# Kernel optimization log

Measured on AMD Instinct MI355X. Metric: run time of the kernel, lower is better.

## Reference

```python
import jax, jax.numpy as jnp
import numpy as np

B, N, DIM = 4, 2048, 512
H, DH = 8, 64  # n_heads, dim_head; inner = H*DH = 512
SCALE = DH ** -0.5


def setup_inputs() -> dict:
    key = jax.random.key(0)
    k1, k2, k3 = jax.random.split(key, 3)
    inner = H * DH
    X = jax.random.normal(k1, (B, N, DIM), dtype=jnp.float32)
    W_qkv = jax.random.normal(k2, (DIM, 3 * inner), dtype=jnp.float32) * (DIM ** -0.5)
    W_out = jax.random.normal(k3, (inner, DIM), dtype=jnp.float32) * (inner ** -0.5)
    b_out = jnp.zeros((DIM,), dtype=jnp.float32)
    return {"X": X, "W_qkv": W_qkv, "W_out": W_out, "b_out": b_out}


def reference(X, W_qkv, W_out, b_out):
    # X: (b, n, dim)
    qkv = X @ W_qkv                      # (b, n, 3*h*d)
    q, k, v = jnp.split(qkv, 3, axis=-1)
    def to_heads(t):
        b, n, _ = t.shape
        return t.reshape(b, n, H, DH).transpose(0, 2, 1, 3)  # (b, h, n, d)
    q, k, v = to_heads(q), to_heads(k), to_heads(v)
    # NOTE: original computes scores[n, m] = k_n . q_m and softmaxes over m (query axis)
    scores = jnp.einsum('bhnd,bhmd->bhnm', k, q) * SCALE     # (b, h, n_k, m_q)
    att = jax.nn.softmax(scores, axis=-1)
    # out token axis is the KEY index n: out[n, d] = sum_e att[n, e] * v[e, d]
    out = jnp.einsum('bhne,bhed->bhnd', att, v)              # (b, h, n, d)
    out = out.transpose(0, 2, 1, 3).reshape(X.shape[0], X.shape[1], H * DH)  # (b, n, h*d)
    return out @ W_out + b_out
```

## Files before the change

### kernel.cpp

```cpp
#include <hip/hip_runtime.h>
#include <hip/hip_bf16.h>

typedef __bf16 bf16_t;
typedef bf16_t bf16x8 __attribute__((ext_vector_type(8)));
typedef bf16_t bf16x4v __attribute__((ext_vector_type(4)));
typedef float f32x4 __attribute__((ext_vector_type(4)));
typedef float f32x16 __attribute__((ext_vector_type(16)));
typedef int i32x4 __attribute__((ext_vector_type(4)));

#define B_SZ 4
#define N_TOK 2048
#define DIM 512
#define H_N 8
#define DH 64
#define INNER 512
#define M_ROWS 8192
#define NQKV 1536
#define K_FOLD 0.18033688011112042f

#define GLD_LDS16(gp, lp)                                          \
  __builtin_amdgcn_global_load_lds(                                \
      (const __attribute__((address_space(1))) void*)(gp),         \
      (__attribute__((address_space(3))) void*)(lp), 16, 0, 0)

__device__ __forceinline__ float fexp2(float x) {
#if __has_builtin(__builtin_amdgcn_exp2f)
  return __builtin_amdgcn_exp2f(x);
#else
  float r;
  asm volatile("v_exp_f32 %0, %1\n\ts_nop 1" : "=v"(r) : "v"(x));
  return r;
#endif
}

__device__ __forceinline__ int cvtpk_bf16(float lo, float hi) {
  int r;
  asm("v_cvt_pk_bf16_f32 %0, %1, %2" : "=v"(r) : "v"(lo), "v"(hi));
  return r;
}

__device__ __forceinline__ void permswap32(int& a, int& b) {
  asm volatile("v_permlane32_swap_b32 %0, %1" : "+v"(a), "+v"(b));
}


__global__ void f32_to_bf16_kernel(const float* __restrict__ src,
                                   bf16_t* __restrict__ dst, int n4) {
  int i = blockIdx.x * blockDim.x + threadIdx.x;
  int stride = gridDim.x * blockDim.x;
  for (; i < n4; i += stride) {
    float4 f = reinterpret_cast<const float4*>(src)[i];
    bf16x4v o;
    o.x = (bf16_t)f.x; o.y = (bf16_t)f.y; o.z = (bf16_t)f.z; o.w = (bf16_t)f.w;
    reinterpret_cast<bf16x4v*>(dst)[i] = o;
  }
}

__global__ void transpose_f32_to_bf16_kernel(const float* __restrict__ src,
                                             bf16_t* __restrict__ dst, int R, int C) {
  int t = blockIdx.x * blockDim.x + threadIdx.x;
  if (t >= R * C) return;
  int r = t / C, c = t - r * C;
  dst[(size_t)c * R + r] = (bf16_t)src[t];
}

template <int MODE>
__global__ __launch_bounds__(256) void gemm_bf16_kernel(
    const bf16_t* __restrict__ A, const bf16_t* __restrict__ Bt,
    int M, int Nn, int K,
    bf16_t* __restrict__ qb, bf16_t* __restrict__ kb, bf16_t* __restrict__ vtb,
    float* __restrict__ outF, const float* __restrict__ bias) {
  __shared__ bf16_t As[128 * 64];
  __shared__ bf16_t Bs[128 * 64];

  const int tid = threadIdx.x;
  const int lane = tid & 63;
  const int wave = tid >> 6;
  const int g = lane >> 4, c = lane & 15;
  const int wm = (wave >> 1) * 64, wn = (wave & 1) * 64;
  const int m0 = blockIdx.x * 128, n0 = blockIdx.y * 128;

  f32x4 acc[4][4] = {};

  for (int k0 = 0; k0 < K; k0 += 64) {
    __syncthreads();
    #pragma unroll
    for (int i = 0; i < 4; ++i) {
      int blk = i * 256 + tid;
      int row = blk >> 3;
      int cb = (blk & 7) ^ (row & 7);
      int base = (i * 256 + wave * 64) * 8;
      GLD_LDS16(A + (size_t)(m0 + row) * K + k0 + cb * 8, &As[base]);
      GLD_LDS16(Bt + (size_t)(n0 + row) * K + k0 + cb * 8, &Bs[base]);
    }
    __syncthreads();
    __builtin_amdgcn_s_setprio(1);
    #pragma unroll
    for (int ks = 0; ks < 2; ++ks) {
      bf16x8 af[4], bfr[4];
      #pragma unroll
      for (int i = 0; i < 4; ++i) {
        af[i] = *reinterpret_cast<const bf16x8*>(
            &As[(wm + i * 16 + c) * 64 + (((ks * 4 + g) ^ (c & 7)) * 8)]);
        bfr[i] = *reinterpret_cast<const bf16x8*>(
            &Bs[(wn + i * 16 + c) * 64 + (((ks * 4 + g) ^ (c & 7)) * 8)]);
      }
      #pragma unroll
      for (int mi = 0; mi < 4; ++mi)
        #pragma unroll
        for (int ni = 0; ni < 4; ++ni)
          acc[mi][ni] = __builtin_amdgcn_mfma_f32_16x16x32_bf16(
              af[mi], bfr[ni], acc[mi][ni], 0, 0, 0);
    }
    __builtin_amdgcn_s_setprio(0);
  }

  #pragma unroll
  for (int mi = 0; mi < 4; ++mi) {
    #pragma unroll
    for (int ni = 0; ni < 4; ++ni) {
      int colg = n0 + wn + ni * 16 + c;
      if (MODE == 0) {
        int s = colg >> 9;
        int hh = (colg >> 6) & 7, dd = colg & 63;
        int rowg0 = m0 + wm + mi * 16 + g * 4;
        int bb = rowg0 >> 11, nn = rowg0 & 2047;
        if (s == 2) {
          bf16x4v pk;
          pk.x = (bf16_t)acc[mi][ni][0];
          pk.y = (bf16_t)acc[mi][ni][1];
          pk.z = (bf16_t)acc[mi][ni][2];
          pk.w = (bf16_t)acc[mi][ni][3];
          *reinterpret_cast<bf16x4v*>(
              &vtb[(((size_t)(bb * H_N + hh)) * DH + dd) * N_TOK + nn]) = pk;
        } else {
          float sc = (s == 1) ? K_FOLD : 1.0f;
          bf16_t* dst = (s == 0) ? qb : kb;
          #pragma unroll
          for (int r = 0; r < 4; ++r)
            dst[(((size_t)(bb * H_N + hh)) * N_TOK + nn + r) * DH + dd] =
                (bf16_t)(acc[mi][ni][r] * sc);
        }
      } else {
        #pragma unroll
        for (int r = 0; r < 4; ++r) {
          int rowg = m0 + wm + mi * 16 + g * 4 + r;
          outF[(size_t)rowg * Nn + colg] = acc[mi][ni][r] + bias[colg];
        }
      }
    }
  }
}

__global__ __launch_bounds__(256, 1) void attn_kernel(
    const bf16_t* __restrict__ Qproj, const bf16_t* __restrict__ Kproj,
    const bf16_t* __restrict__ Vt, bf16_t* __restrict__ att_out) {
  const int glin = blockIdx.x;
  const int xcd = glin & 7;
  const int jj = glin >> 3;
  const int hb = xcd * 4 + (jj >> 3);
  const int rb = jj & 7;
  const int h = hb & 7, b = hb >> 3;

  const size_t hbo = (size_t)(b * H_N + h);
  const bf16_t* Aq = Kproj + hbo * N_TOK * DH;
  const bf16_t* Ak = Qproj + hbo * N_TOK * DH;
  const bf16_t* Av = Vt + hbo * (size_t)DH * N_TOK;

  const int tid = threadIdx.x, lane = tid & 63, wave = tid >> 6;
  const int nl = lane & 31;
  const int hf = lane >> 5;
  const int r0 = rb * 256, wr0 = wave * 64;

  __shared__ bf16_t sK[2][128 * 64];
  __shared__ bf16_t sV[2][64 * 128];

  bf16x8 qreg[2][4];
  #pragma unroll
  for (int cs = 0; cs < 2; ++cs)
    #pragma unroll
    for (int ks = 0; ks < 4; ++ks)
      qreg[cs][ks] = *reinterpret_cast<const bf16x8*>(
          &Aq[(size_t)(r0 + wr0 + cs * 32 + nl) * DH + ks * 16 + hf * 8]);

  f32x16 accO[2][2] = {};
  float Lp[2][2] = {};

  auto stage = [&](bf16_t* dK, bf16_t* dV, int j0) {
    #pragma unroll
    for (int i = 0; i < 4; ++i) {
      int idx = i * 256 + tid;
      int base = (i * 256 + wave * 64) * 8;
      int rowK = idx >> 3;
      int cbK = (idx & 7) ^ (rowK & 7);
      GLD_LDS16(Ak + (size_t)(j0 + rowK) * DH + cbK * 8, dK + base);
      int rowV = idx >> 4;
      int sv = idx & 15;
      int pV = (sv & 8) | ((sv & 7) ^ (rowV & 7));
      GLD_LDS16(Av + (size_t)rowV * N_TOK + j0 + pV * 8, dV + base);
    }
  };

  stage(sK[0], sV[0], 0);
  __syncthreads();

  constexpr int NT = N_TOK / 128;
  for (int t = 0; t < NT; ++t) {
    if (t + 1 < NT) stage(sK[(t + 1) & 1], sV[(t + 1) & 1], (t + 1) * 128);
    const bf16_t* bK = sK[t & 1];
    const bf16_t* bV = sV[t & 1];

    #pragma unroll
    for (int ch = 0; ch < 2; ++ch) {
      f32x16 accT[2][2] = {};
      __builtin_amdgcn_s_setprio(1);
      #pragma unroll
      for (int ks = 0; ks < 4; ++ks) {
        #pragma unroll
        for (int mi = 0; mi < 2; ++mi) {
          int rowt = ch * 64 + mi * 32 + nl;
          bf16x8 ak = *reinterpret_cast<const bf16x8*>(
              &bK[rowt * 64 + (((ks * 2 + hf) ^ (rowt & 7)) * 8)]);
          accT[0][mi] = __builtin_amdgcn_mfma_f32_32x32x16_bf16(
              ak, qreg[0][ks], accT[0][mi], 0, 0, 0);
          accT[1][mi] = __builtin_amdgcn_mfma_f32_32x32x16_bf16(
              ak, qreg[1][ks], accT[1][mi], 0, 0, 0);
        }
      }
      __builtin_amdgcn_s_setprio(0);

      #pragma unroll
      for (int cs = 0; cs < 2; ++cs)
        #pragma unroll
        for (int mi = 0; mi < 2; ++mi)
          #pragma unroll
          for (int r = 0; r < 16; ++r) {
            float p = fexp2(accT[cs][mi][r]);
            accT[cs][mi][r] = p;
            Lp[cs][mi] += p;
          }

      __builtin_amdgcn_s_setprio(1);
      #pragma unroll
      for (int ks = 0; ks < 4; ++ks) {
        bf16x8 av[2];
        #pragma unroll
        for (int vi = 0; vi < 2; ++vi) {
          int rowv = vi * 32 + nl;
          int pp = ch * 8 + ks * 2 + hf;
          av[vi] = *reinterpret_cast<const bf16x8*>(
              &bV[rowv * 128 + (((pp & 8) | ((pp & 7) ^ (rowv & 7))) * 8)]);
        }
        #pragma unroll
        for (int cs = 0; cs < 2; ++cs) {
          const int mi = ks >> 1, base = (ks & 1) * 8;
          int a0 = cvtpk_bf16(accT[cs][mi][base + 0], accT[cs][mi][base + 1]);
          int b0 = cvtpk_bf16(accT[cs][mi][base + 4], accT[cs][mi][base + 5]);
          int a1 = cvtpk_bf16(accT[cs][mi][base + 2], accT[cs][mi][base + 3]);
          int b1 = cvtpk_bf16(accT[cs][mi][base + 6], accT[cs][mi][base + 7]);
          permswap32(a0, b0);
          permswap32(a1, b1);
          i32x4 w; w.x = a0; w.y = a1; w.z = b0; w.w = b1;
          bf16x8 pfrag = __builtin_bit_cast(bf16x8, w);
          accO[cs][0] = __builtin_amdgcn_mfma_f32_32x32x16_bf16(
              av[0], pfrag, accO[cs][0], 0, 0, 0);
          accO[cs][1] = __builtin_amdgcn_mfma_f32_32x32x16_bf16(
              av[1], pfrag, accO[cs][1], 0, 0, 0);
        }
      }
      __builtin_amdgcn_s_setprio(0);
    }

    __syncthreads();
  }

  #pragma unroll
  for (int cs = 0; cs < 2; ++cs) {
    float l = Lp[cs][0] + Lp[cs][1];
    l += __shfl_xor(l, 32);
    float invL = 1.0f / l;
    const int nrow = r0 + wr0 + cs * 32 + nl;
    #pragma unroll
    for (int vi = 0; vi < 2; ++vi) {
      #pragma unroll
      for (int q = 0; q < 4; ++q) {
        int d0 = 32 * vi + 8 * q + 4 * hf;
        bf16x4v o;
        o.x = (bf16_t)(accO[cs][vi][4 * q + 0] * invL);
        o.y = (bf16_t)(accO[cs][vi][4 * q + 1] * invL);
        o.z = (bf16_t)(accO[cs][vi][4 * q + 2] * invL);
        o.w = (bf16_t)(accO[cs][vi][4 * q + 3] * invL);
        *reinterpret_cast<bf16x4v*>(
            &att_out[((size_t)(b * N_TOK) + nrow) * INNER + h * DH + d0]) = o;
      }
    }
  }
}


extern "C" void kernel_launch(void* const* d_in, const int* in_sizes, int n_in,
                              void* d_out, int out_size, void* d_ws, size_t ws_size,
                              hipStream_t stream) {
  const float* X    = (const float*)d_in[0];
  const float* Wqkv = (const float*)d_in[1];
  const float* Wout = (const float*)d_in[2];
  const float* bout = (const float*)d_in[3];
  float* out = (float*)d_out;

  char* ws = (char*)d_ws;
  bf16_t* Xb    = (bf16_t*)(ws);
  bf16_t* WqkvT = (bf16_t*)(ws + 8388608);
  bf16_t* WoutT = (bf16_t*)(ws + 9961472);
  bf16_t* Qb    = (bf16_t*)(ws + 10485760);
  bf16_t* Kb    = (bf16_t*)(ws + 18874368);
  bf16_t* Vtb   = (bf16_t*)(ws + 27262976);
  bf16_t* AttO  = (bf16_t*)(ws + 35651584);

  f32_to_bf16_kernel<<<2048, 256, 0, stream>>>(X, Xb, (M_ROWS * DIM) / 4);
  transpose_f32_to_bf16_kernel<<<(DIM * NQKV + 255) / 256, 256, 0, stream>>>(
      Wqkv, WqkvT, DIM, NQKV);
  transpose_f32_to_bf16_kernel<<<(INNER * DIM + 255) / 256, 256, 0, stream>>>(
      Wout, WoutT, INNER, DIM);

  dim3 g1(M_ROWS / 128, NQKV / 128);
  gemm_bf16_kernel<0><<<g1, 256, 0, stream>>>(Xb, WqkvT, M_ROWS, NQKV, DIM,
                                              Qb, Kb, Vtb, nullptr, nullptr);

  attn_kernel<<<dim3(256), 256, 0, stream>>>(Qb, Kb, Vtb, AttO);

  dim3 g3(M_ROWS / 128, DIM / 128);
  gemm_bf16_kernel<1><<<g3, 256, 0, stream>>>(AttO, WoutT, M_ROWS, DIM, DIM,
                                              nullptr, nullptr, nullptr, out, bout);
}
```

Before: 98.34 us.

## Halve attention rows per block, double grid, compute softmax denominator via MFMA

Each wave now handles 32 query rows instead of 64, so the grid doubles to 512 blocks and launch bounds allow two blocks per CU. The softmax row sum moves from per-element VALU adds and a shuffle to an extra MFMA against a ones vector, and the exp and pack steps are restructured into separate phases per tile. The goal is more occupancy and latency hiding with fewer VALU ops. The cost is K/V tiles being staged twice as often per query row, plus one extra MFMA per step.

```diff
diff --git a/kernel.cpp b/kernel.cpp
--- a/kernel.cpp
+++ b/kernel.cpp
@@ -152,14 +152,14 @@
   }
 }
 
-__global__ __launch_bounds__(256, 1) void attn_kernel(
+__global__ __launch_bounds__(256, 2) void attn_kernel(
     const bf16_t* __restrict__ Qproj, const bf16_t* __restrict__ Kproj,
     const bf16_t* __restrict__ Vt, bf16_t* __restrict__ att_out) {
   const int glin = blockIdx.x;
   const int xcd = glin & 7;
   const int jj = glin >> 3;
-  const int hb = xcd * 4 + (jj >> 3);
-  const int rb = jj & 7;
+  const int hb = xcd * 4 + (jj >> 4);
+  const int rb = jj & 15;
   const int h = hb & 7, b = hb >> 3;
 
   const size_t hbo = (size_t)(b * H_N + h);
@@ -170,21 +170,23 @@
   const int tid = threadIdx.x, lane = tid & 63, wave = tid >> 6;
   const int nl = lane & 31;
   const int hf = lane >> 5;
-  const int r0 = rb * 256, wr0 = wave * 64;
+  const int r0 = rb * 128, wr0 = wave * 32;
 
   __shared__ bf16_t sK[2][128 * 64];
   __shared__ bf16_t sV[2][64 * 128];
 
-  bf16x8 qreg[2][4];
+  bf16x8 qreg[4];
   #pragma unroll
-  for (int cs = 0; cs < 2; ++cs)
-    #pragma unroll
-    for (int ks = 0; ks < 4; ++ks)
-      qreg[cs][ks] = *reinterpret_cast<const bf16x8*>(
-          &Aq[(size_t)(r0 + wr0 + cs * 32 + nl) * DH + ks * 16 + hf * 8]);
-
-  f32x16 accO[2][2] = {};
-  float Lp[2][2] = {};
+  for (int ks = 0; ks < 4; ++ks)
+    qreg[ks] = *reinterpret_cast<const bf16x8*>(
+        &Aq[(size_t)(r0 + wr0 + nl) * DH + ks * 16 + hf * 8]);
+
+  bf16x8 ones;
+  #pragma unroll
+  for (int i = 0; i < 8; ++i) ones[i] = (bf16_t)1.0f;
+
+  f32x16 accO0 = {}, accO1 = {};
+  f32x16 accL = {};
 
   auto stage = [&](bf16_t* dK, bf16_t* dV, int j0) {
     #pragma unroll
@@ -210,10 +212,10 @@
     const bf16_t* bK = sK[t & 1];
     const bf16_t* bV = sV[t & 1];
 
+    f32x16 aT[2][2] = {};
+    __builtin_amdgcn_s_setprio(1);
     #pragma unroll
     for (int ch = 0; ch < 2; ++ch) {
-      f32x16 accT[2][2] = {};
-      __builtin_amdgcn_s_setprio(1);
       #pragma unroll
       for (int ks = 0; ks < 4; ++ks) {
         #pragma unroll
@@ -221,79 +223,78 @@
           int rowt = ch * 64 + mi * 32 + nl;
           bf16x8 ak = *reinterpret_cast<const bf16x8*>(
               &bK[rowt * 64 + (((ks * 2 + hf) ^ (rowt & 7)) * 8)]);
-          accT[0][mi] = __builtin_amdgcn_mfma_f32_32x32x16_bf16(
-              ak, qreg[0][ks], accT[0][mi], 0, 0, 0);
-          accT[1][mi] = __builtin_amdgcn_mfma_f32_32x32x16_bf16(
-              ak, qreg[1][ks], accT[1][mi], 0, 0, 0);
+          aT[ch][mi] = __builtin_amdgcn_mfma_f32_32x32x16_bf16(
+              ak, qreg[ks], aT[ch][mi], 0, 0, 0);
         }
       }
-      __builtin_amdgcn_s_setprio(0);
-
-      #pragma unroll
-      for (int cs = 0; cs < 2; ++cs)
+    }
+    __builtin_amdgcn_s_setprio(0);
+
+    #pragma unroll
+    for (int ch = 0; ch < 2; ++ch)
+      #pragma unroll
+      for (int mi = 0; mi < 2; ++mi)
         #pragma unroll
-        for (int mi = 0; mi < 2; ++mi)
-          #pragma unroll
-          for (int r = 0; r < 16; ++r) {
-            float p = fexp2(accT[cs][mi][r]);
-            accT[cs][mi][r] = p;
-            Lp[cs][mi] += p;
-          }
-
-      __builtin_amdgcn_s_setprio(1);
+        for (int r = 0; r < 16; ++r)
+          aT[ch][mi][r] = fexp2(aT[ch][mi][r]);
+
+    i32x4 pk[2][4];
+    #pragma unroll
+    for (int ch = 0; ch < 2; ++ch) {
       #pragma unroll
       for (int ks = 0; ks < 4; ++ks) {
-        bf16x8 av[2];
-        #pragma unroll
-        for (int vi = 0; vi < 2; ++vi) {
-          int rowv = vi * 32 + nl;
-          int pp = ch * 8 + ks * 2 + hf;
-          av[vi] = *reinterpret_cast<const bf16x8*>(
-              &bV[rowv * 128 + (((pp & 8) | ((pp & 7) ^ (rowv & 7))) * 8)]);
-        }
-        #pragma unroll
-        for (int cs = 0; cs < 2; ++cs) {
-          const int mi = ks >> 1, base = (ks & 1) * 8;
-          int a0 = cvtpk_bf16(accT[cs][mi][base + 0], accT[cs][mi][base + 1]);
-          int b0 = cvtpk_bf16(accT[cs][mi][base + 4], accT[cs][mi][base + 5]);
-          int a1 = cvtpk_bf16(accT[cs][mi][base + 2], accT[cs][mi][base + 3]);
-          int b1 = cvtpk_bf16(accT[cs][mi][base + 6], accT[cs][mi][base + 7]);
-          permswap32(a0, b0);
-          permswap32(a1, b1);
-          i32x4 w; w.x = a0; w.y = a1; w.z = b0; w.w = b1;
-          bf16x8 pfrag = __builtin_bit_cast(bf16x8, w);
-          accO[cs][0] = __builtin_amdgcn_mfma_f32_32x32x16_bf16(
-              av[0], pfrag, accO[cs][0], 0, 0, 0);
-          accO[cs][1] = __builtin_amdgcn_mfma_f32_32x32x16_bf16(
-              av[1], pfrag, accO[cs][1], 0, 0, 0);
-        }
-      }
-      __builtin_amdgcn_s_setprio(0);
-    }
+        const int mi = ks >> 1, base = (ks & 1) * 8;
+        int a0 = cvtpk_bf16(aT[ch][mi][base + 0], aT[ch][mi][base + 1]);
+        int b0 = cvtpk_bf16(aT[ch][mi][base + 4], aT[ch][mi][base + 5]);
+        int a1 = cvtpk_bf16(aT[ch][mi][base + 2], aT[ch][mi][base + 3]);
+        int b1 = cvtpk_bf16(aT[ch][mi][base + 6], aT[ch][mi][base + 7]);
+        permswap32(a0, b0);
+        permswap32(a1, b1);
+        pk[ch][ks].x = a0; pk[ch][ks].y = a1; pk[ch][ks].z = b0; pk[ch][ks].w = b1;
+      }
+    }
+
+    __builtin_amdgcn_s_setprio(1);
+    #pragma unroll
+    for (int ch = 0; ch < 2; ++ch) {
+      #pragma unroll
+      for (int ks = 0; ks < 4; ++ks) {
+        bf16x8 pfrag = __builtin_bit_cast(bf16x8, pk[ch][ks]);
+        int pp = ch * 8 + ks * 2 + hf;
+        int rv0 = nl, rv1 = 32 + nl;
+        bf16x8 av0 = *reinterpret_cast<const bf16x8*>(
+            &bV[rv0 * 128 + (((pp & 8) | ((pp & 7) ^ (rv0 & 7))) * 8)]);
+        bf16x8 av1 = *reinterpret_cast<const bf16x8*>(
+            &bV[rv1 * 128 + (((pp & 8) | ((pp & 7) ^ (rv1 & 7))) * 8)]);
+        accO0 = __builtin_amdgcn_mfma_f32_32x32x16_bf16(av0, pfrag, accO0, 0, 0, 0);
+        accO1 = __builtin_amdgcn_mfma_f32_32x32x16_bf16(av1, pfrag, accO1, 0, 0, 0);
+        accL  = __builtin_amdgcn_mfma_f32_32x32x16_bf16(ones, pfrag, accL, 0, 0, 0);
+      }
+    }
+    __builtin_amdgcn_s_setprio(0);
 
     __syncthreads();
   }
 
+  float invL = 1.0f / accL[0];
+  const int nrow = r0 + wr0 + nl;
   #pragma unroll
-  for (int cs = 0; cs < 2; ++cs) {
-    float l = Lp[cs][0] + Lp[cs][1];
-    l += __shfl_xor(l, 32);
-    float invL = 1.0f / l;
-    const int nrow = r0 + wr0 + cs * 32 + nl;
-    #pragma unroll
-    for (int vi = 0; vi < 2; ++vi) {
-      #pragma unroll
-      for (int q = 0; q < 4; ++q) {
-        int d0 = 32 * vi + 8 * q + 4 * hf;
-        bf16x4v o;
-        o.x = (bf16_t)(accO[cs][vi][4 * q + 0] * invL);
-        o.y = (bf16_t)(accO[cs][vi][4 * q + 1] * invL);
-        o.z = (bf16_t)(accO[cs][vi][4 * q + 2] * invL);
-        o.w = (bf16_t)(accO[cs][vi][4 * q + 3] * invL);
-        *reinterpret_cast<bf16x4v*>(
-            &att_out[((size_t)(b * N_TOK) + nrow) * INNER + h * DH + d0]) = o;
-      }
-    }
+  for (int q = 0; q < 4; ++q) {
+    int d0a = 8 * q + 4 * hf;
+    bf16x4v o;
+    o.x = (bf16_t)(accO0[4 * q + 0] * invL);
+    o.y = (bf16_t)(accO0[4 * q + 1] * invL);
+    o.z = (bf16_t)(accO0[4 * q + 2] * invL);
+    o.w = (bf16_t)(accO0[4 * q + 3] * invL);
+    *reinterpret_cast<bf16x4v*>(
+        &att_out[((size_t)(b * N_TOK) + nrow) * INNER + h * DH + d0a]) = o;
+    bf16x4v o2;
+    o2.x = (bf16_t)(accO1[4 * q + 0] * invL);
+    o2.y = (bf16_t)(accO1[4 * q + 1] * invL);
+    o2.z = (bf16_t)(accO1[4 * q + 2] * invL);
+    o2.w = (bf16_t)(accO1[4 * q + 3] * invL);
+    *reinterpret_cast<bf16x4v*>(
+        &att_out[((size_t)(b * N_TOK) + nrow) * INNER + h * DH + 32 + d0a]) = o2;
   }
 }
 
@@ -326,7 +327,7 @@
   gemm_bf16_kernel<0><<<g1, 256, 0, stream>>>(Xb, WqkvT, M_ROWS, NQKV, DIM,
                                               Qb, Kb, Vtb, nullptr, nullptr);
 
-  attn_kernel<<<dim3(256), 256, 0, stream>>>(Qb, Kb, Vtb, AttO);
+  attn_kernel<<<dim3(512), 256, 0, stream>>>(Qb, Kb, Vtb, AttO);
 
   dim3 g3(M_ROWS / 128, DIM / 128);
   gemm_bf16_kernel<1><<<g3, 256, 0, stream>>>(AttO, WoutT, M_ROWS, DIM, DIM,
```

After: 93.08 us. 5.3% less time.
